# Kernel tuning notes

Measured on AMD Instinct MI355X. Metric: run time of the kernel, lower is better.

The kernel has to match this reference:

```python
import jax, jax.numpy as jnp
import numpy as np
import math

D = 1024
H = 16
HD = D // H

def layernorm(x, g, b, eps=1e-5):
    mu = jnp.mean(x, axis=-1, keepdims=True)
    var = jnp.var(x, axis=-1, keepdims=True)
    return (x - mu) * jax.lax.rsqrt(var + eps) * g + b

def setup_inputs() -> dict:
    key = jax.random.key(0)
    ks = jax.random.split(key, 12)
    s = 0.02
    return {
        "x": jax.random.normal(ks[0], (2, 2048, D), jnp.float32),
        "Wk": jax.random.normal(ks[1], (D, D), jnp.float32) * s,
        "Wq": jax.random.normal(ks[2], (D, D), jnp.float32) * s,
        "Wv": jax.random.normal(ks[3], (D, D), jnp.float32) * s,
        "Wp": jax.random.normal(ks[4], (D, D), jnp.float32) * s,
        "bp": jnp.zeros((D,), jnp.float32),
        "g1": jnp.ones((D,), jnp.float32),
        "b1": jnp.zeros((D,), jnp.float32),
        "g2": jnp.ones((D,), jnp.float32),
        "b2": jnp.zeros((D,), jnp.float32),
        "W1": jax.random.normal(ks[5], (D, 4 * D), jnp.float32) * s,
        "bm1": jnp.zeros((4 * D,), jnp.float32),
        "W2": jax.random.normal(ks[6], (4 * D, D), jnp.float32) * s,
        "bm2": jnp.zeros((D,), jnp.float32),
    }

def reference(x, Wk, Wq, Wv, Wp, bp, g1, b1, g2, b2, W1, bm1, W2, bm2):
    B, S, _ = x.shape
    xn = layernorm(x, g1, b1)  # pre-LN; residual uses xn (faithful to source)
    # project and split heads -> [B, H, S, HD]
    def heads(y):
        return y.reshape(B, S, H, HD).transpose(0, 2, 1, 3)
    q = heads(xn @ Wq)
    k = heads(xn @ Wk)
    v = heads(xn @ Wv)
    scale = 1.0 / math.sqrt(HD)
    att = jnp.einsum('bhsd,bhtd->bhst', q, k) * scale  # [B,H,S,S]
    diag = jnp.eye(S, dtype=bool)
    att = jnp.where(diag, -jnp.inf, att)  # exclude self-attention on diagonal
    att = jax.nn.softmax(att, axis=-1)
    y = jnp.einsum('bhst,bhtd->bhsd', att, v)
    y = y.transpose(0, 2, 1, 3).reshape(B, S, D)
    y = y @ Wp + bp  # dropout is identity at inference
    h = xn + y
    hn = layernorm(h, g2, b2)
    mlp = jax.nn.gelu(hn @ W1 + bm1, approximate=False) @ W2 + bm2
    return h + mlp
```

## Files before the change

### kernel.cpp

```cpp
#include <hip/hip_runtime.h>
#include <hip/hip_bf16.h>
#include <math.h>

#define BATCH   2
#define SEQ     2048
#define D_MODEL 1024
#define NHEAD   16
#define HEADD   64
#define NROWS   (BATCH * SEQ)
#define D_FF    4096
#define TPARTS  4
#define TSPAN   (SEQ / TPARTS)

typedef __bf16 bf16_t;
typedef __bf16 bf16x2 __attribute__((ext_vector_type(2)));
typedef __bf16 bf16x4 __attribute__((ext_vector_type(4)));
typedef __bf16 bf16x8 __attribute__((ext_vector_type(8)));
typedef float  f32x4  __attribute__((ext_vector_type(4)));

#define QSCALE 0.18033688011112042f

__device__ __forceinline__ void gload_lds16(const void* g, void* l) {
    __builtin_amdgcn_global_load_lds(
        (const __attribute__((address_space(1))) unsigned int*)g,
        (__attribute__((address_space(3))) unsigned int*)l, 16, 0, 0);
}

__global__ __launch_bounds__(256) void transpose_all6(
    const float* __restrict__ Wq, const float* __restrict__ Wk,
    const float* __restrict__ Wv, const float* __restrict__ Wp,
    const float* __restrict__ W1, const float* __restrict__ W2,
    bf16_t* __restrict__ Wqkvt, bf16_t* __restrict__ Wpt,
    bf16_t* __restrict__ W1t, bf16_t* __restrict__ W2t)
{
    __shared__ float tile[32][33];
    int bid = blockIdx.x;
    const float* W; bf16_t* Wt; int K, N, n0, k0;
    if (bid < 4096) {
        int seg = bid >> 10, t = bid & 1023;
        W  = (seg == 0) ? Wq : (seg == 1) ? Wk : (seg == 2) ? Wv : Wp;
        Wt = (seg < 3) ? (Wqkvt + (size_t)seg * 1024 * 1024) : Wpt;
        K = 1024; N = 1024;
        n0 = (t & 31) * 32; k0 = (t >> 5) * 32;
    } else if (bid < 8192) {
        int t = bid - 4096;
        W = W1; Wt = W1t; K = 1024; N = 4096;
        n0 = (t & 127) * 32; k0 = (t >> 7) * 32;
    } else {
        int t = bid - 8192;
        W = W2; Wt = W2t; K = 4096; N = 1024;
        n0 = (t & 31) * 32; k0 = (t >> 5) * 32;
    }
    int tx = threadIdx.x;
    int ty = threadIdx.y;
    #pragma unroll
    for (int i = 0; i < 32; i += 8)
        tile[ty + i][tx] = W[(size_t)(k0 + ty + i) * N + n0 + tx];
    __syncthreads();
    #pragma unroll
    for (int i = 0; i < 32; i += 8)
        Wt[(size_t)(n0 + ty + i) * K + k0 + tx] = (bf16_t)tile[tx][ty + i];
}

__global__ __launch_bounds__(256) void ln_kernel(
    const float* __restrict__ x, const float* __restrict__ g,
    const float* __restrict__ b, bf16_t* __restrict__ out)
{
    int row = blockIdx.x;
    int tid = threadIdx.x;
    const float* xr = x + (size_t)row * D_MODEL;
    f32x4 v = *(const f32x4*)(xr + tid * 4);
    float s  = v[0] + v[1] + v[2] + v[3];
    float s2 = v[0]*v[0] + v[1]*v[1] + v[2]*v[2] + v[3]*v[3];
    #pragma unroll
    for (int off = 32; off; off >>= 1) {
        s  += __shfl_down(s, off);
        s2 += __shfl_down(s2, off);
    }
    __shared__ float ps[4], ps2[4];
    int w = tid >> 6, lane = tid & 63;
    if (lane == 0) { ps[w] = s; ps2[w] = s2; }
    __syncthreads();
    float sum  = ps[0] + ps[1] + ps[2] + ps[3];
    float sum2 = ps2[0] + ps2[1] + ps2[2] + ps2[3];
    float mu  = sum * (1.0f / D_MODEL);
    float var = sum2 * (1.0f / D_MODEL) - mu * mu;
    float rs  = rsqrtf(var + 1e-5f);
    #pragma unroll
    for (int j = 0; j < 4; ++j) {
        int c = tid * 4 + j;
        out[(size_t)row * D_MODEL + c] = (bf16_t)((v[j] - mu) * rs * g[c] + b[c]);
    }
}

template<int EPI>
__global__ __launch_bounds__(512) void gemm256(
    const bf16_t* __restrict__ A, const bf16_t* __restrict__ Bt,
    const float* __restrict__ bias, void* __restrict__ out,
    int M, int N, int K)
{
    __shared__ bf16_t As[2][256 * 64];
    __shared__ bf16_t Bs[2][256 * 64];
    int tid = threadIdx.x;
    int bid = blockIdx.x;
    int m0 = (bid & 15) * 256;
    int n0 = (bid >> 4) * 256;
    int w = tid >> 6, lane = tid & 63, quad = lane >> 4, l15 = lane & 15;
    int wm = (w >> 2) * 128;
    int wn = (w & 3) * 64;
    int rxs = l15 & 7;

    int srow = tid >> 3;
    int sxor = (((tid & 7) ^ (srow & 7)) << 3);
    const bf16_t* Ap = A  + (size_t)(m0 + srow) * K + sxor;
    const bf16_t* Bp = Bt + (size_t)(n0 + srow) * K + sxor;

    f32x4 acc[8][4] = {};

    int nt = K >> 6;
    {
        bf16_t* AsW = &As[0][w * 512];
        bf16_t* BsW = &Bs[0][w * 512];
        #pragma unroll
        for (int h = 0; h < 2; ++h)
            #pragma unroll
            for (int p = 0; p < 2; ++p) {
                gload_lds16(Ap + (size_t)(h * 128 + p * 64) * K, AsW + h * 8192 + p * 4096);
                gload_lds16(Bp + (size_t)(h * 128 + p * 64) * K, BsW + h * 8192 + p * 4096);
            }
    }

    for (int t = 0; t < nt; ++t) {
        int cur = t & 1;
        const bf16_t* Asc = &As[cur][0];
        const bf16_t* Bsc = &Bs[cur][0];
        bf16_t* AsN = &As[cur ^ 1][w * 512];
        bf16_t* BsN = &Bs[cur ^ 1][w * 512];
        bool pf = (t + 1 < nt);
        int k1 = (t + 1) << 6;
        asm volatile("s_waitcnt vmcnt(0)" ::: "memory");
        __builtin_amdgcn_s_barrier();
        __builtin_amdgcn_sched_barrier(0);

        bf16x8 bfr[4][2];
        #pragma unroll
        for (int q = 0; q < 4; ++q) {
            bf16x8 af[2][2];
            #pragma unroll
            for (int ii = 0; ii < 2; ++ii)
                #pragma unroll
                for (int kk = 0; kk < 2; ++kk)
                    af[ii][kk] = *(const bf16x8*)&Asc[(wm + (2 * q + ii) * 16 + l15) * 64
                                                      + (((kk * 4 + quad) ^ rxs) << 3)];
            if (q == 0) {
                #pragma unroll
                for (int j = 0; j < 4; ++j)
                    #pragma unroll
                    for (int kk = 0; kk < 2; ++kk)
                        bfr[j][kk] = *(const bf16x8*)&Bsc[(wn + j * 16 + l15) * 64
                                                          + (((kk * 4 + quad) ^ rxs) << 3)];
            }
            if (q == 0 && pf) {
                #pragma unroll
                for (int h = 0; h < 2; ++h)
                    #pragma unroll
                    for (int p = 0; p < 2; ++p)
                        gload_lds16(Ap + (size_t)(h * 128 + p * 64) * K + k1,
                                    AsN + h * 8192 + p * 4096);
            }
            if (q == 1 && pf) {
                #pragma unroll
                for (int h = 0; h < 2; ++h)
                    #pragma unroll
                    for (int p = 0; p < 2; ++p)
                        gload_lds16(Bp + (size_t)(h * 128 + p * 64) * K + k1,
                                    BsN + h * 8192 + p * 4096);
            }
            #pragma unroll
            for (int ii = 0; ii < 2; ++ii)
                #pragma unroll
                for (int j = 0; j < 4; ++j)
                    #pragma unroll
                    for (int kk = 0; kk < 2; ++kk)
                        acc[2 * q + ii][j] = __builtin_amdgcn_mfma_f32_16x16x32_bf16(
                            af[ii][kk], bfr[j][kk], acc[2 * q + ii][j], 0, 0, 0);
        }
    }

    #pragma unroll
    for (int i = 0; i < 8; ++i)
    #pragma unroll
    for (int j = 0; j < 4; ++j) {
        int col  = n0 + wn + j * 16 + l15;
        int row0 = m0 + wm + i * 16 + quad * 4;
        if (EPI == 6) {
            int region = (n0 + wn + j * 16) >> 10;
            if (region < 2) {
                #pragma unroll
                for (int r = 0; r < 4; ++r) {
                    int row = row0 + r;
                    float v = acc[i][j][r];
                    if (region == 0) v *= QSCALE;
                    int b = row >> 11, s = row & 2047, hh = (col & 1023) >> 6, d = col & 63;
                    bf16_t* dst = (bf16_t*)out + (size_t)region * 4194304;
                    dst[(((size_t)(b * NHEAD + hh)) * SEQ + s) * HEADD + d] = (bf16_t)v;
                }
            } else {
                int dg = col - 2048, hh = dg >> 6, d = dg & 63;
                int b = row0 >> 11, s0 = row0 & 2047;
                bf16x4 pv;
                #pragma unroll
                for (int r = 0; r < 4; ++r) pv[r] = (bf16_t)acc[i][j][r];
                *(bf16x4*)((bf16_t*)out + 8388608
                           + (((size_t)(b * NHEAD + hh)) * HEADD + d) * SEQ + s0) = pv;
            }
        } else {
            float bv = bias[col];
            #pragma unroll
            for (int r = 0; r < 4; ++r) {
                int row = row0 + r;
                float u = acc[i][j][r] + bv;
                float y = u * (0.7978845608028654f + 0.03567740814f * u * u);
                float e = __builtin_amdgcn_exp2f(2.8853900817779268f * y);
                float r8 = __builtin_amdgcn_rcpf(e + 1.0f);
                ((bf16_t*)out)[(size_t)row * N + col] = (bf16_t)(u - u * r8);
            }
        }
    }
}

template<int EPI>
__global__ __launch_bounds__(256) void gemm128(
    const bf16_t* __restrict__ A, const bf16_t* __restrict__ Bt,
    const float* __restrict__ bias, const void* __restrict__ resid,
    void* __restrict__ out, int M, int N, int K, int RY)
{
    __shared__ bf16_t As[3][128 * 64];
    __shared__ bf16_t Bs[3][64 * 64];
    int tid = threadIdx.x;
    int bid = blockIdx.x;
    int cx = bid & 3, cy = (bid >> 2) & 1, i0 = bid >> 3;
    int m0 = ((cx << 3) + (i0 & 7)) << 7;
    int n0 = (cy * RY + (i0 >> 3)) * 64;
    int w = tid >> 6, lane = tid & 63, quad = lane >> 4, l15 = lane & 15;
    int wm = (w & 1) * 64, wn = (w >> 1) * 32;
    int srow = tid >> 3;
    int sxor = (((tid & 7) ^ (srow & 7)) << 3);

    const bf16_t* Ap = A  + (size_t)(m0 + srow) * K + sxor;
    const bf16_t* Bp = Bt + (size_t)(n0 + srow) * K + sxor;

    int rxs = l15 & 7;

    auto stage = [&](int buf, int k0) {
        bf16_t* AsW = &As[buf][w * 512];
        bf16_t* BsW = &Bs[buf][w * 512];
        #pragma unroll
        for (int p = 0; p < 4; ++p)
            gload_lds16(Ap + (size_t)p * 32 * K + k0, AsW + p * 2048);
        #pragma unroll
        for (int p = 0; p < 2; ++p)
            gload_lds16(Bp + (size_t)p * 32 * K + k0, BsW + p * 2048);
    };

    f32x4 acc[4][2] = {};

    int nt = K >> 6;
    stage(0, 0);
    if (nt > 1) stage(1, 64);
    for (int t = 0; t < nt; ++t) {
        int cur = t % 3;
        if (t + 1 < nt) asm volatile("s_waitcnt vmcnt(6)" ::: "memory");
        else            asm volatile("s_waitcnt vmcnt(0)" ::: "memory");
        __builtin_amdgcn_s_barrier();
        __builtin_amdgcn_sched_barrier(0);
        if (t + 2 < nt) stage((t + 2) % 3, (t + 2) << 6);
        #pragma unroll
        for (int kk = 0; kk < 2; ++kk) {
            bf16x8 af[4], bfr[2];
            #pragma unroll
            for (int i = 0; i < 4; ++i)
                af[i] = *(const bf16x8*)&As[cur][(wm + i * 16 + l15) * 64
                                            + ((((kk << 2) | quad) ^ rxs) << 3)];
            #pragma unroll
            for (int j = 0; j < 2; ++j)
                bfr[j] = *(const bf16x8*)&Bs[cur][(wn + j * 16 + l15) * 64
                                            + ((((kk << 2) | quad) ^ rxs) << 3)];
            #pragma unroll
            for (int i = 0; i < 4; ++i)
                #pragma unroll
                for (int j = 0; j < 2; ++j)
                    acc[i][j] = __builtin_amdgcn_mfma_f32_16x16x32_bf16(af[i], bfr[j], acc[i][j], 0, 0, 0);
        }
    }

    #pragma unroll
    for (int i = 0; i < 4; ++i)
    #pragma unroll
    for (int j = 0; j < 2; ++j) {
        int col  = n0 + wn + j * 16 + l15;
        int row0 = m0 + wm + i * 16 + quad * 4;
        float bv = bias[col];
        #pragma unroll
        for (int r = 0; r < 4; ++r) {
            int row = row0 + r;
            float vacc = acc[i][j][r] + bv;
            if (EPI == 1) {
                float res = (float)((const bf16_t*)resid)[(size_t)row * N + col];
                ((float*)out)[(size_t)row * N + col] = vacc + res;
            } else {
                float res = ((const float*)resid)[(size_t)row * N + col];
                ((float*)out)[(size_t)row * N + col] = vacc + res;
            }
        }
    }
}

__global__ __launch_bounds__(256, 4) void attn_kernel(
    const bf16_t* __restrict__ q, const bf16_t* __restrict__ k,
    const bf16_t* __restrict__ vt, bf16_t* __restrict__ po,
    float* __restrict__ plsum)
{
    int gid = blockIdx.x;
    int xcd = gid & 7;
    int loc = gid >> 3;
    int bh  = xcd * 4 + (loc >> 6);
    int rest = loc & 63;
    int qt   = rest >> 2;
    int part = rest & 3;
    int tb0 = part * TSPAN, tend = tb0 + TSPAN;
    int b = bh >> 4, h = bh & 15;
    int tid = threadIdx.x, w = tid >> 6, lane = tid & 63;
    int quad = lane >> 4, l15 = lane & 15;
    int qbase = qt * 128 + w * 32;
    const bf16_t* qh = q  + (size_t)bh * SEQ * HEADD;
    const bf16_t* kh = k  + (size_t)bh * SEQ * HEADD;
    const bf16_t* vh = vt + (size_t)bh * HEADD * SEQ;

    bf16x8 qa[2][2];
    #pragma unroll
    for (int m = 0; m < 2; ++m)
        #pragma unroll
        for (int hf = 0; hf < 2; ++hf)
            qa[m][hf] = *(const bf16x8*)(qh + (size_t)(qbase + m * 16 + l15) * HEADD + hf * 32 + quad * 8);

    bf16x8 ones;
    #pragma unroll
    for (int j = 0; j < 8; ++j) ones[j] = (bf16_t)1.0f;

    __shared__ alignas(16) bf16_t Ks[32 * 72];
    __shared__ alignas(16) bf16_t Vs[64 * 40];
    __shared__ alignas(16) bf16_t Pl[4][32][40];

    int ksrow = tid >> 3, kscol = (tid & 7) * 8;
    int vsrow = tid >> 2, vscol = (tid & 3) * 8;
    const bf16_t* kg = kh + (size_t)ksrow * HEADD + kscol;
    const bf16_t* vg = vh + (size_t)vsrow * SEQ + vscol;

    f32x4 o[2][4] = {};
    f32x4 ls[2] = {};

    for (int t0 = tb0; t0 < tend; t0 += 32) {
        bf16x8 kreg = *(const bf16x8*)(kg + (size_t)t0 * HEADD);
        bf16x8 vreg = *(const bf16x8*)(vg + t0);
        __syncthreads();
        *(bf16x8*)&Ks[ksrow * 72 + kscol] = kreg;
        *(bf16x8*)&Vs[vsrow * 40 + vscol] = vreg;
        __syncthreads();

        bf16x8 kb[2][2], vf[4];
        #pragma unroll
        for (int jt = 0; jt < 2; ++jt)
            #pragma unroll
            for (int hf = 0; hf < 2; ++hf)
                kb[jt][hf] = *(const bf16x8*)&Ks[(2 * l15 + jt) * 72 + hf * 32 + quad * 8];
        #pragma unroll
        for (int dn = 0; dn < 4; ++dn)
            vf[dn] = *(const bf16x8*)&Vs[(dn * 16 + l15) * 40 + quad * 8];

        #pragma unroll
        for (int m = 0; m < 2; ++m) {
            f32x4 sc[2];
            #pragma unroll
            for (int jt = 0; jt < 2; ++jt) {
                f32x4 z = {};
                z = __builtin_amdgcn_mfma_f32_16x16x32_bf16(qa[m][0], kb[jt][0], z, 0, 0, 0);
                z = __builtin_amdgcn_mfma_f32_16x16x32_bf16(qa[m][1], kb[jt][1], z, 0, 0, 0);
                sc[jt] = z;
            }
            int qm = qbase + m * 16;
            bool dg = (t0 < qm + 16) && (t0 + 32 > qm);
            #pragma unroll
            for (int r = 0; r < 4; ++r) {
                int qrow = qm + quad * 4 + r;
                float p0 = __builtin_amdgcn_exp2f(sc[0][r]);
                float p1 = __builtin_amdgcn_exp2f(sc[1][r]);
                if (dg) {
                    int tg = t0 + 2 * l15;
                    if (tg == qrow)     p0 = 0.0f;
                    if (tg + 1 == qrow) p1 = 0.0f;
                }
                bf16x2 pp = { (bf16_t)p0, (bf16_t)p1 };
                *(bf16x2*)&Pl[w][m * 16 + quad * 4 + r][2 * l15] = pp;
            }
        }
        #pragma unroll
        for (int m = 0; m < 2; ++m) {
            bf16x8 pf = *(const bf16x8*)&Pl[w][m * 16 + l15][quad * 8];
            ls[m] = __builtin_amdgcn_mfma_f32_16x16x32_bf16(pf, ones, ls[m], 0, 0, 0);
            #pragma unroll
            for (int dn = 0; dn < 4; ++dn)
                o[m][dn] = __builtin_amdgcn_mfma_f32_16x16x32_bf16(pf, vf[dn], o[m][dn], 0, 0, 0);
        }
    }

    #pragma unroll
    for (int m = 0; m < 2; ++m)
        #pragma unroll
        for (int dn = 0; dn < 4; ++dn)
            #pragma unroll
            for (int r = 0; r < 4; ++r) {
                int qrow = qbase + m * 16 + quad * 4 + r;
                po[(((size_t)part * NROWS) + b * SEQ + qrow) * D_MODEL
                   + h * HEADD + dn * 16 + l15] = (bf16_t)o[m][dn][r];
            }
    if (l15 == 0) {
        #pragma unroll
        for (int m = 0; m < 2; ++m)
            #pragma unroll
            for (int r = 0; r < 4; ++r) {
                int qrow = qbase + m * 16 + quad * 4 + r;
                plsum[((size_t)part * 32 + bh) * SEQ + qrow] = ls[m][r];
            }
    }
}

__global__ __launch_bounds__(256) void attn_merge(
    const bf16_t* __restrict__ po, const float* __restrict__ plsum,
    bf16_t* __restrict__ y)
{
    int row = blockIdx.x;
    int tid = threadIdx.x;
    int c = tid * 4;
    int b = row >> 11, s = row & 2047;
    int bh = b * NHEAD + (c >> 6);
    float l = 0.0f;
    f32x4 ov = {};
    #pragma unroll
    for (int p = 0; p < TPARTS; ++p) {
        l += plsum[((size_t)p * 32 + bh) * SEQ + s];
        bf16x4 t = *(const bf16x4*)&po[((size_t)p * NROWS + row) * D_MODEL + c];
        #pragma unroll
        for (int j = 0; j < 4; ++j) ov[j] += (float)t[j];
    }
    float rl = 1.0f / l;
    bf16x4 out;
    #pragma unroll
    for (int j = 0; j < 4; ++j) out[j] = (bf16_t)(ov[j] * rl);
    *(bf16x4*)&y[(size_t)row * D_MODEL + c] = out;
}

extern "C" void kernel_launch(void* const* d_in, const int* in_sizes, int n_in,
                              void* d_out, int out_size, void* d_ws, size_t ws_size,
                              hipStream_t stream)
{
    const float* x   = (const float*)d_in[0];
    const float* Wk  = (const float*)d_in[1];
    const float* Wq  = (const float*)d_in[2];
    const float* Wv  = (const float*)d_in[3];
    const float* Wp  = (const float*)d_in[4];
    const float* bp  = (const float*)d_in[5];
    const float* g1  = (const float*)d_in[6];
    const float* b1  = (const float*)d_in[7];
    const float* g2  = (const float*)d_in[8];
    const float* b2  = (const float*)d_in[9];
    const float* W1  = (const float*)d_in[10];
    const float* bm1 = (const float*)d_in[11];
    const float* W2  = (const float*)d_in[12];
    const float* bm2 = (const float*)d_in[13];

    char* ws = (char*)d_ws;
    const size_t MB = 1024 * 1024;
    bf16_t* Wqkvt = (bf16_t*)(ws + 0 * MB);
    bf16_t* Wpt = (bf16_t*)(ws + 6 * MB);
    bf16_t* W1t = (bf16_t*)(ws + 8 * MB);
    bf16_t* W2t = (bf16_t*)(ws + 16 * MB);
    bf16_t* xn  = (bf16_t*)(ws + 24 * MB);
    bf16_t* qkv = (bf16_t*)(ws + 32 * MB);
    bf16_t* qb  = (bf16_t*)(ws + 32 * MB);
    bf16_t* kb  = (bf16_t*)(ws + 40 * MB);
    bf16_t* vtb = (bf16_t*)(ws + 48 * MB);
    bf16_t* yb  = (bf16_t*)(ws + 56 * MB);
    float*  hbuf= (float*) (ws + 64 * MB);
    bf16_t* po  = (bf16_t*)(ws + 64 * MB);
    float*  pls = (float*) (ws + 96 * MB);
    bf16_t* hn  = (bf16_t*)(ws + 24 * MB);
    bf16_t* act = (bf16_t*)(ws + 32 * MB);

    transpose_all6<<<12288, dim3(32, 8), 0, stream>>>(
        Wq, Wk, Wv, Wp, W1, W2, Wqkvt, Wpt, W1t, W2t);

    ln_kernel<<<NROWS, 256, 0, stream>>>(x, g1, b1, xn);

    gemm256<6><<<192, 512, 0, stream>>>(xn, Wqkvt, nullptr, qkv, NROWS, 3072, D_MODEL);

    attn_kernel<<<2048, 256, 0, stream>>>(qb, kb, vtb, po, pls);
    attn_merge<<<NROWS, 256, 0, stream>>>(po, pls, yb);

    gemm128<1><<<512, 256, 0, stream>>>(yb, Wpt, bp, xn, hbuf, NROWS, D_MODEL, D_MODEL, 8);

    ln_kernel<<<NROWS, 256, 0, stream>>>(hbuf, g2, b2, hn);

    gemm256<2><<<256, 512, 0, stream>>>(hn, W1t, bm1, act, NROWS, D_FF, D_MODEL);
    gemm128<3><<<512, 256, 0, stream>>>(act, W2t, bm2, hbuf, d_out, NROWS, D_MODEL, D_FF, 8);
}
```

Before: 332.4 us.

## Replace 128x64 GEMM with 128x128 tile, 512-thread, K=128 double-buffered kernel

Replaces the 128x64-tile, 256-thread, triple-buffered GEMM used for the output projection and the second MLP GEMM with a square 128x128-tile kernel. It uses 8 waves and a K-step of 128 with double buffering, and the next-stage loads are interleaved between the two halves of the MFMA work. This gives more reuse per loaded tile and fewer grid blocks, but halves the block count to 256 and raises LDS per block to 128KB. Blocks are mapped with plain row-major ordering, and the earlier grouped rasterization is dropped. A full vmcnt(0) wait each iteration may expose load latency.

```diff
diff --git a/kernel.cpp b/kernel.cpp
--- a/kernel.cpp
+++ b/kernel.cpp
@@ -230,67 +230,87 @@
 }
 
 template<int EPI>
-__global__ __launch_bounds__(256) void gemm128(
+__global__ __launch_bounds__(512) void gemm128sq(
     const bf16_t* __restrict__ A, const bf16_t* __restrict__ Bt,
     const float* __restrict__ bias, const void* __restrict__ resid,
-    void* __restrict__ out, int M, int N, int K, int RY)
-{
-    __shared__ bf16_t As[3][128 * 64];
-    __shared__ bf16_t Bs[3][64 * 64];
+    void* __restrict__ out, int M, int N, int K)
+{
+    __shared__ bf16_t As[2][128 * 128];
+    __shared__ bf16_t Bs[2][128 * 128];
     int tid = threadIdx.x;
     int bid = blockIdx.x;
-    int cx = bid & 3, cy = (bid >> 2) & 1, i0 = bid >> 3;
-    int m0 = ((cx << 3) + (i0 & 7)) << 7;
-    int n0 = (cy * RY + (i0 >> 3)) * 64;
+    int m0 = (bid & 31) * 128;
+    int n0 = (bid >> 5) * 128;
     int w = tid >> 6, lane = tid & 63, quad = lane >> 4, l15 = lane & 15;
-    int wm = (w & 1) * 64, wn = (w >> 1) * 32;
-    int srow = tid >> 3;
-    int sxor = (((tid & 7) ^ (srow & 7)) << 3);
-
+    int wm = (w >> 2) * 64;
+    int wn = (w & 3) * 32;
+    int rxs = l15 & 7;
+
+    int srow = tid >> 4;
+    int sxor = (((tid & 15) ^ (srow & 7)) << 3);
     const bf16_t* Ap = A  + (size_t)(m0 + srow) * K + sxor;
     const bf16_t* Bp = Bt + (size_t)(n0 + srow) * K + sxor;
 
-    int rxs = l15 & 7;
-
-    auto stage = [&](int buf, int k0) {
-        bf16_t* AsW = &As[buf][w * 512];
-        bf16_t* BsW = &Bs[buf][w * 512];
-        #pragma unroll
-        for (int p = 0; p < 4; ++p)
-            gload_lds16(Ap + (size_t)p * 32 * K + k0, AsW + p * 2048);
-        #pragma unroll
-        for (int p = 0; p < 2; ++p)
-            gload_lds16(Bp + (size_t)p * 32 * K + k0, BsW + p * 2048);
-    };
-
     f32x4 acc[4][2] = {};
-
-    int nt = K >> 6;
-    stage(0, 0);
-    if (nt > 1) stage(1, 64);
+    int nt = K >> 7;
+
+    {
+        bf16_t* AsW = &As[0][w * 512];
+        bf16_t* BsW = &Bs[0][w * 512];
+        #pragma unroll
+        for (int p = 0; p < 4; ++p) {
+            gload_lds16(Ap + (size_t)p * 32 * K, AsW + p * 4096);
+            gload_lds16(Bp + (size_t)p * 32 * K, BsW + p * 4096);
+        }
+    }
+
     for (int t = 0; t < nt; ++t) {
-        int cur = t % 3;
-        if (t + 1 < nt) asm volatile("s_waitcnt vmcnt(6)" ::: "memory");
-        else            asm volatile("s_waitcnt vmcnt(0)" ::: "memory");
+        int cur = t & 1;
+        const bf16_t* Asc = &As[cur][0];
+        const bf16_t* Bsc = &Bs[cur][0];
+        bf16_t* AsN = &As[cur ^ 1][w * 512];
+        bf16_t* BsN = &Bs[cur ^ 1][w * 512];
+        bool pf = (t + 1 < nt);
+        int k1 = (t + 1) << 7;
+        asm volatile("s_waitcnt vmcnt(0)" ::: "memory");
         __builtin_amdgcn_s_barrier();
         __builtin_amdgcn_sched_barrier(0);
-        if (t + 2 < nt) stage((t + 2) % 3, (t + 2) << 6);
-        #pragma unroll
-        for (int kk = 0; kk < 2; ++kk) {
-            bf16x8 af[4], bfr[2];
-            #pragma unroll
-            for (int i = 0; i < 4; ++i)
-                af[i] = *(const bf16x8*)&As[cur][(wm + i * 16 + l15) * 64
-                                            + ((((kk << 2) | quad) ^ rxs) << 3)];
-            #pragma unroll
-            for (int j = 0; j < 2; ++j)
-                bfr[j] = *(const bf16x8*)&Bs[cur][(wn + j * 16 + l15) * 64
-                                            + ((((kk << 2) | quad) ^ rxs) << 3)];
-            #pragma unroll
-            for (int i = 0; i < 4; ++i)
+
+        bf16x8 bfr[2][4];
+        #pragma unroll
+        for (int half = 0; half < 2; ++half) {
+            bf16x8 af[2][4];
+            #pragma unroll
+            for (int ii = 0; ii < 2; ++ii)
+                #pragma unroll
+                for (int kk = 0; kk < 4; ++kk)
+                    af[ii][kk] = *(const bf16x8*)&Asc[(wm + (2 * half + ii) * 16 + l15) * 128
+                                                      + (((kk * 4 + quad) ^ rxs) << 3)];
+            if (half == 0) {
                 #pragma unroll
                 for (int j = 0; j < 2; ++j)
-                    acc[i][j] = __builtin_amdgcn_mfma_f32_16x16x32_bf16(af[i], bfr[j], acc[i][j], 0, 0, 0);
+                    #pragma unroll
+                    for (int kk = 0; kk < 4; ++kk)
+                        bfr[j][kk] = *(const bf16x8*)&Bsc[(wn + j * 16 + l15) * 128
+                                                          + (((kk * 4 + quad) ^ rxs) << 3)];
+                if (pf) {
+                    #pragma unroll
+                    for (int p = 0; p < 4; ++p)
+                        gload_lds16(Ap + (size_t)p * 32 * K + k1, AsN + p * 4096);
+                }
+            } else if (pf) {
+                #pragma unroll
+                for (int p = 0; p < 4; ++p)
+                    gload_lds16(Bp + (size_t)p * 32 * K + k1, BsN + p * 4096);
+            }
+            #pragma unroll
+            for (int ii = 0; ii < 2; ++ii)
+                #pragma unroll
+                for (int j = 0; j < 2; ++j)
+                    #pragma unroll
+                    for (int kk = 0; kk < 4; ++kk)
+                        acc[2 * half + ii][j] = __builtin_amdgcn_mfma_f32_16x16x32_bf16(
+                            af[ii][kk], bfr[j][kk], acc[2 * half + ii][j], 0, 0, 0);
         }
     }
 
@@ -507,10 +527,10 @@
     attn_kernel<<<2048, 256, 0, stream>>>(qb, kb, vtb, po, pls);
     attn_merge<<<NROWS, 256, 0, stream>>>(po, pls, yb);
 
-    gemm128<1><<<512, 256, 0, stream>>>(yb, Wpt, bp, xn, hbuf, NROWS, D_MODEL, D_MODEL, 8);
+    gemm128sq<1><<<256, 512, 0, stream>>>(yb, Wpt, bp, xn, hbuf, NROWS, D_MODEL, D_MODEL);
 
     ln_kernel<<<NROWS, 256, 0, stream>>>(hbuf, g2, b2, hn);
 
     gemm256<2><<<256, 512, 0, stream>>>(hn, W1t, bm1, act, NROWS, D_FF, D_MODEL);
-    gemm128<3><<<512, 256, 0, stream>>>(act, W2t, bm2, hbuf, d_out, NROWS, D_MODEL, D_FF, 8);
-}
+    gemm128sq<3><<<256, 512, 0, stream>>>(act, W2t, bm2, hbuf, d_out, NROWS, D_MODEL, D_FF);
+}
```

New measurement: 322.4 us. 1.03x faster.
